# Kernel optimization log

Measured on AMD Instinct MI355X. Metric: run time of the kernel, lower is better.

Reference implementation:

```python
import jax, jax.numpy as jnp
import numpy as np


def squash(t, axis=-1):
    # scale = |t|^2/(1+|t|^2) ; out = scale * t/|t|  (matches torch version incl. no eps)
    sn = jnp.sum(t * t, axis=axis, keepdims=True)
    return sn / (1.0 + sn) * t / jnp.sqrt(sn)


def setup_inputs() -> dict:
    key = jax.random.key(0)
    ks = jax.random.split(key, 6)
    B = 512
    return {
        "x": jax.random.normal(ks[0], (B, 1, 28, 28), jnp.float32),
        "conv_w": jax.random.normal(ks[1], (256, 1, 9, 9), jnp.float32) * 0.05,
        "conv_b": jax.random.normal(ks[2], (256,), jnp.float32) * 0.05,
        # 8 primary-capsule convs Conv2d(256,32,9,9,stride=2) stacked on output channels
        "prim_w": jax.random.normal(ks[3], (8 * 32, 256, 9, 9), jnp.float32) * 0.02,
        "prim_b": jax.random.normal(ks[4], (8 * 32,), jnp.float32) * 0.02,
        # route_weights: (num_capsules=10, num_route_nodes=1152, input_dim=8, output_dim=16)
        "route_w": jax.random.normal(ks[5], (10, 1152, 8, 16), jnp.float32),
    }


def reference(x, conv_w, conv_b, prim_w, prim_b, route_w):
    B = x.shape[0]
    dn = ("NCHW", "OIHW", "NCHW")
    # stem: 1->256, k9 s1, no activation in original code
    y = jax.lax.conv_general_dilated(x, conv_w, (1, 1), "VALID", dimension_numbers=dn)
    y = y + conv_b[None, :, None, None]                      # [B,256,20,20]
    # primary caps: 8 parallel convs 256->32, k9 s2, fused into one conv
    p = jax.lax.conv_general_dilated(y, prim_w, (2, 2), "VALID", dimension_numbers=dn)
    p = p + prim_b[None, :, None, None]                      # [B,256,6,6]
    p = p.reshape(B, 8, 32 * 6 * 6)                          # per-capsule flatten (C,H,W)
    u = squash(jnp.transpose(p, (0, 2, 1)))                  # [B,1152,8]
    # priors[b,c,r,o] = u[b,r,:] @ route_w[c,r,:,:]
    priors = jnp.einsum("bri,crio->bcro", u, route_w)        # [B,10,1152,16]
    blog = jnp.zeros((B, 10, 1152), priors.dtype)
    v = None
    for _ in range(3):  # num_iterations = 3 (fixed)
        probs = jax.nn.softmax(blog, axis=2)[..., None]      # softmax over route dim
        v = squash(jnp.sum(priors * probs, axis=2, keepdims=True))  # [B,10,1,16]
        blog = blog + jnp.sum(priors * v, axis=-1)           # agreement update
    v = v[:, :, 0, :]                                        # [B,10,16]
    logits = jnp.sqrt(jnp.sum(v * v, axis=-1))               # capsule lengths
    return jax.nn.softmax(logits, axis=-1)                   # [B,10]
```

## Files before the change

### kernel.cpp

```cpp
#include <hip/hip_runtime.h>
#include <cstddef>
#include <cstdint>

typedef _Float16 f16;
typedef _Float16 f16x4 __attribute__((ext_vector_type(4)));
typedef _Float16 f16x8 __attribute__((ext_vector_type(8)));
typedef float f32x4 __attribute__((ext_vector_type(4)));
typedef float f32x16 __attribute__((ext_vector_type(16)));

#define AS1 __attribute__((address_space(1)))
#define AS3 __attribute__((address_space(3)))


__device__ __forceinline__ float wave_max(float v) {
#pragma unroll
  for (int m = 1; m < 64; m <<= 1) v = fmaxf(v, __shfl_xor(v, m, 64));
  return v;
}
__device__ __forceinline__ float wave_sum(float v) {
#pragma unroll
  for (int m = 1; m < 64; m <<= 1) v += __shfl_xor(v, m, 64);
  return v;
}

__global__ __launch_bounds__(256) void conv1_kernel(
    const float* __restrict__ x, const float* __restrict__ w,
    const float* __restrict__ bias, f16* __restrict__ y16) {
  const int b   = blockIdx.x;
  const int oc0 = blockIdx.y * 64;
  const int t   = threadIdx.x;
  const int tx  = t & 15;
  const int ty  = t >> 4;
  const int oxg = ty & 3;
  const int oy0 = ty >> 2;

  __shared__ float x_s[784];
  __shared__ float w_s[81][68];

  for (int idx = t; idx < 784; idx += 256) x_s[idx] = x[b * 784 + idx];
  for (int idx = t; idx < 64 * 81; idx += 256) {
    const int oc_l = idx / 81, k = idx % 81;
    w_s[k][oc_l] = w[(oc0 + oc_l) * 81 + k];
  }
  __syncthreads();

  float bz[4];
#pragma unroll
  for (int j = 0; j < 4; ++j) bz[j] = bias[oc0 + tx * 4 + j];

  for (int m = 0; m < 5; ++m) {
    const int oy = oy0 + m * 4;
    float acc[4][5];
#pragma unroll
    for (int j = 0; j < 4; ++j)
#pragma unroll
      for (int pp = 0; pp < 5; ++pp) acc[j][pp] = 0.f;

#pragma unroll
    for (int ky = 0; ky < 9; ++ky) {
      float xv[13];
      const int base = (oy + ky) * 28 + oxg * 5;
#pragma unroll
      for (int jj = 0; jj < 13; ++jj) xv[jj] = x_s[base + jj];
#pragma unroll
      for (int kx = 0; kx < 9; ++kx) {
        const float4 w4 = *reinterpret_cast<const float4*>(&w_s[ky * 9 + kx][tx * 4]);
#pragma unroll
        for (int pp = 0; pp < 5; ++pp) {
          const float xval = xv[kx + pp];
          acc[0][pp] += w4.x * xval;
          acc[1][pp] += w4.y * xval;
          acc[2][pp] += w4.z * xval;
          acc[3][pp] += w4.w * xval;
        }
      }
    }
#pragma unroll
    for (int pp = 0; pp < 5; ++pp) {
      f16x4 st;
#pragma unroll
      for (int j = 0; j < 4; ++j) st[j] = (f16)(acc[j][pp] + bz[j]);
      const int px = oy * 20 + oxg * 5 + pp;
      *(f16x4*)&y16[((size_t)b * 400 + px) * 256 + oc0 + tx * 4] = st;
    }
  }
}

__global__ __launch_bounds__(256) void wprep_kernel(const float* __restrict__ w,
                                                    f16* __restrict__ w16) {
  const int idx = blockIdx.x * 256 + threadIdx.x;
  const int kk  = idx >> 13;
  const int rem = idx & 8191;
  const int oc  = rem >> 5;
  const int icg = rem & 31;
  f16x8 v;
#pragma unroll
  for (int j = 0; j < 8; ++j)
    v[j] = (f16)w[((size_t)(oc * 256 + icg * 8 + j)) * 81 + kk];
  *(f16x8*)&w16[((size_t)kk * 256 + oc) * 256 + icg * 8] = v;
}

__global__ __launch_bounds__(256, 2) void conv2_mfma(
    const f16* __restrict__ y16, const f16* __restrict__ w16,
    float* __restrict__ p4) {
  const int h       = blockIdx.x;
  const int ntile   = h % 144;
  const int variant = h / 144;
  const int mtile   = variant >> 2;
  const int ks      = variant & 3;
  const int oc0     = mtile * 128;
  const int cicb    = ks * 64;

  const int tid  = threadIdx.x;
  const int lane = tid & 63;
  const int wave = tid >> 6;
  const int l31  = lane & 31;
  const int hi   = lane >> 5;
  const int wm   = wave >> 1;
  const int wn   = wave & 1;

  __shared__ char smem[65536];

  const int lr   = lane >> 3;
  const int swz  = ((lane & 7) ^ (lr & 7)) * 8;
  const f16* aPtr[4];
  uint32_t aLoff[4];
#pragma unroll
  for (int q = 0; q < 4; ++q) {
    const int g  = wave * 4 + q;
    const int oc = oc0 + g * 8 + lr;
    aPtr[q]  = w16 + (size_t)oc * 256 + cicb + swz;
    aLoff[q] = (uint32_t)__builtin_amdgcn_readfirstlane(g * 1024);
  }
  const f16* bPtr[4];
  uint32_t bLoff[4];
#pragma unroll
  for (int q = 0; q < 4; ++q) {
    const int g  = wave * 4 + q;
    const int n  = ntile * 128 + g * 8 + lr;
    const int b  = n / 36;
    const int op = n - b * 36;
    const int oy = op / 6;
    const int ox = op - oy * 6;
    bPtr[q]  = y16 + ((size_t)b * 400 + 40 * oy + 2 * ox) * 256 + cicb + swz;
    bLoff[q] = (uint32_t)__builtin_amdgcn_readfirstlane(16384 + g * 1024);
  }

  f32x16 acc00, acc01, acc10, acc11;
#pragma unroll
  for (int r = 0; r < 16; ++r) {
    acc00[r] = 0.f; acc01[r] = 0.f; acc10[r] = 0.f; acc11[r] = 0.f;
  }

  auto stage = [&](int bb, int kkn) {
    const int ky    = kkn / 9;
    const int kx    = kkn - ky * 9;
    const int koffB = (20 * ky + kx) * 256;
    const size_t koffA = (size_t)kkn * 65536;
#pragma unroll
    for (int q = 0; q < 4; ++q)
      __builtin_amdgcn_global_load_lds(
          (const AS1 uint32_t*)(aPtr[q] + koffA),
          (AS3 uint32_t*)((AS3 char*)smem + bb + aLoff[q]), 16, 0, 0);
#pragma unroll
    for (int q = 0; q < 4; ++q)
      __builtin_amdgcn_global_load_lds(
          (const AS1 uint32_t*)(bPtr[q] + koffB),
          (AS3 uint32_t*)((AS3 char*)smem + bb + bLoff[q]), 16, 0, 0);
  };

  const int rowA  = (wm * 64 + l31) * 128;
  const int rowB  = 16384 + (wn * 64 + l31) * 128;
  const int sbase = l31 & 7;

  stage(0, 0);

  for (int kk = 0; kk < 81; ++kk) {
    const int cur = (kk & 1) * 32768;
    if (kk < 80) {
      stage(cur ^ 32768, kk + 1);
      asm volatile("s_waitcnt vmcnt(8)" ::: "memory");
    } else {
      asm volatile("s_waitcnt vmcnt(0)" ::: "memory");
    }
    __builtin_amdgcn_s_barrier();

    const char* bufp = smem + cur;
    __builtin_amdgcn_s_setprio(1);
#pragma unroll
    for (int kc = 0; kc < 4; ++kc) {
      const int sw = (((kc * 2 + hi) ^ sbase) << 4);
      const f16x8 a0 = *(const f16x8*)(bufp + rowA + sw);
      const f16x8 a1 = *(const f16x8*)(bufp + rowA + 32 * 128 + sw);
      const f16x8 b0 = *(const f16x8*)(bufp + rowB + sw);
      const f16x8 b1 = *(const f16x8*)(bufp + rowB + 32 * 128 + sw);
      acc00 = __builtin_amdgcn_mfma_f32_32x32x16_f16(a0, b0, acc00, 0, 0, 0);
      acc01 = __builtin_amdgcn_mfma_f32_32x32x16_f16(a0, b1, acc01, 0, 0, 0);
      acc10 = __builtin_amdgcn_mfma_f32_32x32x16_f16(a1, b0, acc10, 0, 0, 0);
      acc11 = __builtin_amdgcn_mfma_f32_32x32x16_f16(a1, b1, acc11, 0, 0, 0);
    }
    __builtin_amdgcn_s_setprio(0);
    __builtin_amdgcn_s_barrier();
  }

  float* pk = p4 + (size_t)ks * 4718592;
#pragma unroll
  for (int af = 0; af < 2; ++af) {
#pragma unroll
    for (int bf = 0; bf < 2; ++bf) {
      const f32x16 a = af ? (bf ? acc11 : acc10) : (bf ? acc01 : acc00);
      const int n  = ntile * 128 + wn * 64 + bf * 32 + l31;
      const int b  = n / 36;
      const int op = n - b * 36;
      float* pb = pk + (size_t)b * 9216 + op;
      const int ocb = oc0 + wm * 64 + af * 32 + 4 * hi;
#pragma unroll
      for (int r = 0; r < 16; ++r) {
        const int oc = ocb + (r & 3) + 8 * (r >> 2);
        pb[oc * 36] = a[r];
      }
    }
  }
}

__global__ __launch_bounds__(256) void squash_kernel(const float* __restrict__ p4,
                                                     const float* __restrict__ bias,
                                                     float* __restrict__ u) {
  const int idx = blockIdx.x * 256 + threadIdx.x;
  if (idx >= 512 * 1152) return;
  const int b = idx / 1152;
  const int r = idx % 1152;
  const int c2 = r / 36;
  const int s  = r % 36;
  const size_t base = (size_t)b * 9216 + c2 * 36 + s;
  float tv[8];
  float sn = 0.f;
#pragma unroll
  for (int g = 0; g < 8; ++g) {
    const size_t off = base + (size_t)g * 32 * 36;
    float t = p4[off] + p4[off + 4718592] + p4[off + 2 * 4718592] +
              p4[off + 3 * 4718592] + bias[g * 32 + c2];
    tv[g] = t;
    sn += t * t;
  }
  const float scale = sn / ((1.f + sn) * sqrtf(sn));
  float* up = u + (size_t)idx * 8;
#pragma unroll
  for (int g = 0; g < 8; ++g) up[g] = tv[g] * scale;
}

__global__ __launch_bounds__(256) void routing_kernel(const float* __restrict__ u,
                                                      const float* __restrict__ rw,
                                                      float* __restrict__ logits) {
  const int b    = blockIdx.x;
  const int c    = blockIdx.y;
  const int t    = threadIdx.x;
  const int og   = t & 3;
  const int rg   = t >> 2;
  const int lane = t & 63;
  const int wid  = t >> 6;

  __shared__ float u_s[1152 * 9];
  __shared__ float blog_s[1152];
  __shared__ float red[8];
  __shared__ float sred[64];

  for (int idx = t; idx < 1152 * 8; idx += 256)
    u_s[(idx >> 3) * 9 + (idx & 7)] = u[(size_t)b * 9216 + idx];
  for (int idx = t; idx < 1152; idx += 256) blog_s[idx] = 0.f;
  __syncthreads();

  float pr[18][4];
  const float* rwc = rw + (size_t)c * 1152 * 128;
#pragma unroll
  for (int k = 0; k < 18; ++k) {
    const int r = rg + 64 * k;
    float a0 = 0.f, a1 = 0.f, a2 = 0.f, a3 = 0.f;
#pragma unroll
    for (int i = 0; i < 8; ++i) {
      const float uv = u_s[r * 9 + i];
      const float4 w4 = *reinterpret_cast<const float4*>(rwc + (size_t)r * 128 + i * 16 + og * 4);
      a0 += uv * w4.x; a1 += uv * w4.y; a2 += uv * w4.z; a3 += uv * w4.w;
    }
    pr[k][0] = a0; pr[k][1] = a1; pr[k][2] = a2; pr[k][3] = a3;
  }

  float sn = 0.f;
  float vj[4] = {0.f, 0.f, 0.f, 0.f};

  for (int it = 0; it < 3; ++it) {
    float lmax = -3.4e38f;
    for (int idx = t; idx < 1152; idx += 256) lmax = fmaxf(lmax, blog_s[idx]);
    lmax = wave_max(lmax);
    if (lane == 0) red[wid] = lmax;
    __syncthreads();
    const float gmax = fmaxf(fmaxf(red[0], red[1]), fmaxf(red[2], red[3]));
    float lsum = 0.f;
    for (int idx = t; idx < 1152; idx += 256) lsum += expf(blog_s[idx] - gmax);
    lsum = wave_sum(lsum);
    if (lane == 0) red[4 + wid] = lsum;
    __syncthreads();
    const float ginv = 1.f / (red[4] + red[5] + red[6] + red[7]);

    float sp0 = 0.f, sp1 = 0.f, sp2 = 0.f, sp3 = 0.f;
#pragma unroll
    for (int k = 0; k < 18; ++k) {
      const int r = rg + 64 * k;
      const float pb = expf(blog_s[r] - gmax) * ginv;
      sp0 += pr[k][0] * pb; sp1 += pr[k][1] * pb;
      sp2 += pr[k][2] * pb; sp3 += pr[k][3] * pb;
    }
#pragma unroll
    for (int m = 4; m < 64; m <<= 1) {
      sp0 += __shfl_xor(sp0, m, 64);
      sp1 += __shfl_xor(sp1, m, 64);
      sp2 += __shfl_xor(sp2, m, 64);
      sp3 += __shfl_xor(sp3, m, 64);
    }
    if (lane < 4) {
      sred[wid * 16 + lane * 4 + 0] = sp0;
      sred[wid * 16 + lane * 4 + 1] = sp1;
      sred[wid * 16 + lane * 4 + 2] = sp2;
      sred[wid * 16 + lane * 4 + 3] = sp3;
    }
    __syncthreads();

    sn = 0.f;
#pragma unroll
    for (int o = 0; o < 16; ++o) {
      const float sv = sred[o] + sred[16 + o] + sred[32 + o] + sred[48 + o];
      sn += sv * sv;
    }
    const float scale = sn / ((1.f + sn) * sqrtf(sn));
#pragma unroll
    for (int j = 0; j < 4; ++j) {
      const int o = og * 4 + j;
      vj[j] = (sred[o] + sred[16 + o] + sred[32 + o] + sred[48 + o]) * scale;
    }

    if (it < 2) {
#pragma unroll
      for (int k = 0; k < 18; ++k) {
        float bp = pr[k][0] * vj[0] + pr[k][1] * vj[1] + pr[k][2] * vj[2] + pr[k][3] * vj[3];
        bp += __shfl_xor(bp, 1, 64);
        bp += __shfl_xor(bp, 2, 64);
        if (og == 0) blog_s[rg + 64 * k] += bp;
      }
      __syncthreads();
    }
  }
  if (t == 0) logits[b * 10 + c] = sn / (1.f + sn);
}

__global__ __launch_bounds__(256) void out_softmax_kernel(const float* __restrict__ logits,
                                                          float* __restrict__ out) {
  const int b = blockIdx.x * 256 + threadIdx.x;
  if (b >= 512) return;
  float l[10];
  float mx = -3.4e38f;
#pragma unroll
  for (int cc = 0; cc < 10; ++cc) {
    l[cc] = logits[b * 10 + cc];
    mx = fmaxf(mx, l[cc]);
  }
  float s = 0.f;
#pragma unroll
  for (int cc = 0; cc < 10; ++cc) {
    l[cc] = expf(l[cc] - mx);
    s += l[cc];
  }
  const float inv = 1.f / s;
#pragma unroll
  for (int cc = 0; cc < 10; ++cc) out[b * 10 + cc] = l[cc] * inv;
}

extern "C" void kernel_launch(void* const* d_in, const int* in_sizes, int n_in,
                              void* d_out, int out_size, void* d_ws, size_t ws_size,
                              hipStream_t stream) {
  const float* x       = (const float*)d_in[0];
  const float* conv_w  = (const float*)d_in[1];
  const float* conv_b  = (const float*)d_in[2];
  const float* prim_w  = (const float*)d_in[3];
  const float* prim_b  = (const float*)d_in[4];
  const float* route_w = (const float*)d_in[5];
  float* out = (float*)d_out;

  f16* y16      = (f16*)d_ws;
  f16* w16      = y16 + 52428800;
  float* p4     = (float*)(w16 + 5308416);
  float* u      = p4 + 4 * 4718592;
  float* logits = u + 4718592;

  conv1_kernel<<<dim3(512, 4), 256, 0, stream>>>(x, conv_w, conv_b, y16);
  wprep_kernel<<<2592, 256, 0, stream>>>(prim_w, w16);
  conv2_mfma<<<1152, 256, 0, stream>>>(y16, w16, p4);
  squash_kernel<<<(512 * 1152 + 255) / 256, 256, 0, stream>>>(p4, prim_b, u);
  routing_kernel<<<dim3(512, 10), 256, 0, stream>>>(u, route_w, logits);
  out_softmax_kernel<<<2, 256, 0, stream>>>(logits, out);
}
```

Before: 682.8 us.

## Load conv2 weight fragments directly into registers, halve LDS usage

The weight prep kernel now writes prim weights in an MFMA-fragment-friendly layout (kk, ic-group, oc, 8 ic), so each lane of conv2 can load its A operands straight from global memory into registers, double-buffered across iterations. Only the im2col B tile goes through LDS, which halves shared memory to 32KB and raises the occupancy hint from 2 to 3 blocks per CU. The trade is more VGPR pressure from the two register A buffers and uncached-per-block global weight loads duplicated across the two wn waves.

```diff
diff --git a/kernel.cpp b/kernel.cpp
--- a/kernel.cpp
+++ b/kernel.cpp
@@ -87,21 +87,21 @@
 }
 
 __global__ __launch_bounds__(256) void wprep_kernel(const float* __restrict__ w,
-                                                    f16* __restrict__ w16) {
+                                                    f16* __restrict__ w16t) {
   const int idx = blockIdx.x * 256 + threadIdx.x;
   const int kk  = idx >> 13;
   const int rem = idx & 8191;
-  const int oc  = rem >> 5;
-  const int icg = rem & 31;
+  const int icg = rem >> 8;
+  const int oc  = rem & 255;
   f16x8 v;
 #pragma unroll
   for (int j = 0; j < 8; ++j)
     v[j] = (f16)w[((size_t)(oc * 256 + icg * 8 + j)) * 81 + kk];
-  *(f16x8*)&w16[((size_t)kk * 256 + oc) * 256 + icg * 8] = v;
-}
-
-__global__ __launch_bounds__(256, 2) void conv2_mfma(
-    const f16* __restrict__ y16, const f16* __restrict__ w16,
+  *(f16x8*)&w16t[(((size_t)kk * 32 + icg) * 256 + oc) * 8] = v;
+}
+
+__global__ __launch_bounds__(256, 3) void conv2_mfma(
+    const f16* __restrict__ y16, const f16* __restrict__ w16t,
     float* __restrict__ p4) {
   const int h       = blockIdx.x;
   const int ntile   = h % 144;
@@ -119,19 +119,10 @@
   const int wm   = wave >> 1;
   const int wn   = wave & 1;
 
-  __shared__ char smem[65536];
+  __shared__ char smem[32768];
 
   const int lr   = lane >> 3;
   const int swz  = ((lane & 7) ^ (lr & 7)) * 8;
-  const f16* aPtr[4];
-  uint32_t aLoff[4];
-#pragma unroll
-  for (int q = 0; q < 4; ++q) {
-    const int g  = wave * 4 + q;
-    const int oc = oc0 + g * 8 + lr;
-    aPtr[q]  = w16 + (size_t)oc * 256 + cicb + swz;
-    aLoff[q] = (uint32_t)__builtin_amdgcn_readfirstlane(g * 1024);
-  }
   const f16* bPtr[4];
   uint32_t bLoff[4];
 #pragma unroll
@@ -143,8 +134,10 @@
     const int oy = op / 6;
     const int ox = op - oy * 6;
     bPtr[q]  = y16 + ((size_t)b * 400 + 40 * oy + 2 * ox) * 256 + cicb + swz;
-    bLoff[q] = (uint32_t)__builtin_amdgcn_readfirstlane(16384 + g * 1024);
-  }
+    bLoff[q] = (uint32_t)__builtin_amdgcn_readfirstlane(g * 1024);
+  }
+
+  const int aBase = (ks * 8 + hi) * 2048 + (oc0 + wm * 64 + l31) * 8;
 
   f32x16 acc00, acc01, acc10, acc11;
 #pragma unroll
@@ -156,12 +149,6 @@
     const int ky    = kkn / 9;
     const int kx    = kkn - ky * 9;
     const int koffB = (20 * ky + kx) * 256;
-    const size_t koffA = (size_t)kkn * 65536;
-#pragma unroll
-    for (int q = 0; q < 4; ++q)
-      __builtin_amdgcn_global_load_lds(
-          (const AS1 uint32_t*)(aPtr[q] + koffA),
-          (AS3 uint32_t*)((AS3 char*)smem + bb + aLoff[q]), 16, 0, 0);
 #pragma unroll
     for (int q = 0; q < 4; ++q)
       __builtin_amdgcn_global_load_lds(
@@ -169,36 +156,49 @@
           (AS3 uint32_t*)((AS3 char*)smem + bb + bLoff[q]), 16, 0, 0);
   };
 
-  const int rowA  = (wm * 64 + l31) * 128;
-  const int rowB  = 16384 + (wn * 64 + l31) * 128;
+  auto loadA = [&](f16x8 (&dst)[8], int kkn) {
+    const f16* bp = w16t + (size_t)kkn * 65536 + aBase;
+#pragma unroll
+    for (int kc = 0; kc < 4; ++kc)
+#pragma unroll
+      for (int af = 0; af < 2; ++af)
+        dst[kc * 2 + af] = *(const f16x8*)(bp + kc * 4096 + af * 256);
+  };
+
+  const int rowB  = (wn * 64 + l31) * 128;
   const int sbase = l31 & 7;
 
+  auto compute = [&](const char* bufp, const f16x8 (&aC)[8]) {
+#pragma unroll
+    for (int kc = 0; kc < 4; ++kc) {
+      const int sw = (((kc * 2 + hi) ^ sbase) << 4);
+      const f16x8 b0 = *(const f16x8*)(bufp + rowB + sw);
+      const f16x8 b1 = *(const f16x8*)(bufp + rowB + 32 * 128 + sw);
+      acc00 = __builtin_amdgcn_mfma_f32_32x32x16_f16(aC[kc * 2 + 0], b0, acc00, 0, 0, 0);
+      acc01 = __builtin_amdgcn_mfma_f32_32x32x16_f16(aC[kc * 2 + 0], b1, acc01, 0, 0, 0);
+      acc10 = __builtin_amdgcn_mfma_f32_32x32x16_f16(aC[kc * 2 + 1], b0, acc10, 0, 0, 0);
+      acc11 = __builtin_amdgcn_mfma_f32_32x32x16_f16(aC[kc * 2 + 1], b1, acc11, 0, 0, 0);
+    }
+  };
+
+  f16x8 aA[8], aB[8];
   stage(0, 0);
+  loadA(aA, 0);
 
   for (int kk = 0; kk < 81; ++kk) {
-    const int cur = (kk & 1) * 32768;
+    const char* bufp = smem + (kk & 1) * 16384;
     if (kk < 80) {
-      stage(cur ^ 32768, kk + 1);
-      asm volatile("s_waitcnt vmcnt(8)" ::: "memory");
+      stage((kk & 1) ? 0 : 16384, kk + 1);
+      if (kk & 1) loadA(aA, kk + 1); else loadA(aB, kk + 1);
+      __builtin_amdgcn_sched_barrier(0);
+      asm volatile("s_waitcnt vmcnt(12)" ::: "memory");
     } else {
       asm volatile("s_waitcnt vmcnt(0)" ::: "memory");
     }
     __builtin_amdgcn_s_barrier();
 
-    const char* bufp = smem + cur;
     __builtin_amdgcn_s_setprio(1);
-#pragma unroll
-    for (int kc = 0; kc < 4; ++kc) {
-      const int sw = (((kc * 2 + hi) ^ sbase) << 4);
-      const f16x8 a0 = *(const f16x8*)(bufp + rowA + sw);
-      const f16x8 a1 = *(const f16x8*)(bufp + rowA + 32 * 128 + sw);
-      const f16x8 b0 = *(const f16x8*)(bufp + rowB + sw);
-      const f16x8 b1 = *(const f16x8*)(bufp + rowB + 32 * 128 + sw);
-      acc00 = __builtin_amdgcn_mfma_f32_32x32x16_f16(a0, b0, acc00, 0, 0, 0);
-      acc01 = __builtin_amdgcn_mfma_f32_32x32x16_f16(a0, b1, acc01, 0, 0, 0);
-      acc10 = __builtin_amdgcn_mfma_f32_32x32x16_f16(a1, b0, acc10, 0, 0, 0);
-      acc11 = __builtin_amdgcn_mfma_f32_32x32x16_f16(a1, b1, acc11, 0, 0, 0);
-    }
+    if (kk & 1) compute(bufp, aB); else compute(bufp, aA);
     __builtin_amdgcn_s_setprio(0);
     __builtin_amdgcn_s_barrier();
   }
@@ -386,14 +386,14 @@
   float* out = (float*)d_out;
 
   f16* y16      = (f16*)d_ws;
-  f16* w16      = y16 + 52428800;
-  float* p4     = (float*)(w16 + 5308416);
+  f16* w16t     = y16 + 52428800;
+  float* p4     = (float*)(w16t + 5308416);
   float* u      = p4 + 4 * 4718592;
   float* logits = u + 4718592;
 
   conv1_kernel<<<dim3(512, 4), 256, 0, stream>>>(x, conv_w, conv_b, y16);
-  wprep_kernel<<<2592, 256, 0, stream>>>(prim_w, w16);
-  conv2_mfma<<<1152, 256, 0, stream>>>(y16, w16, p4);
+  wprep_kernel<<<2592, 256, 0, stream>>>(prim_w, w16t);
+  conv2_mfma<<<1152, 256, 0, stream>>>(y16, w16t, p4);
   squash_kernel<<<(512 * 1152 + 255) / 256, 256, 0, stream>>>(p4, prim_b, u);
   routing_kernel<<<dim3(512, 10), 256, 0, stream>>>(u, route_w, logits);
   out_softmax_kernel<<<2, 256, 0, stream>>>(logits, out);
```

After: 2.641 ms. +286.8%, slower.
